# Kernel optimization log

Measured on AMD Instinct MI355X. Metric: run time of the kernel, lower is better.

Reference implementation:

```python
import jax, jax.numpy as jnp
import numpy as np

P_MIN = 0.8        # minimum cumulative probability mass kept per row
THRESHOLD = 1e-10  # drop matches with probability below this
EPS = 1e-6         # distance clamp (matches dist.clamp(min=1e-6) in backward)

B, N, M, D = 4, 4096, 4096, 3


def setup_inputs() -> dict:
    key = jax.random.key(0)
    kx, ky = jax.random.split(key)
    x = jax.random.normal(kx, (B, N, D), dtype=jnp.float32)
    y = jax.random.normal(ky, (B, M, D), dtype=jnp.float32)
    return {"x": x, "y": y}


def _pairwise_dist(x, y):
    # ||x_i - y_j|| via Gram trick; avoids materializing [B,N,M,D] diff tensor.
    sq = (
        jnp.sum(x * x, axis=-1)[:, :, None]
        + jnp.sum(y * y, axis=-1)[:, None, :]
        - 2.0 * jnp.einsum("bnd,bmd->bnm", x, y)
    )
    return jnp.sqrt(jnp.maximum(sq, EPS * EPS))  # [B, N, M]


def _sparse_match_weights(d):
    # Row-wise soft matching probabilities over targets j.
    p = jax.nn.softmax(-d, axis=-1)  # [B, N, M]
    # Keep the most-probable entries per row until cumulative mass reaches P_MIN
    # (the dense, jit-friendly equivalent of the COO compaction in the kernel).
    order = jnp.argsort(-p, axis=-1)
    p_sorted = jnp.take_along_axis(p, order, axis=-1)
    csum = jnp.cumsum(p_sorted, axis=-1)
    keep_sorted = (csum - p_sorted) < P_MIN  # include entry that crosses P_MIN
    inv = jnp.argsort(order, axis=-1)
    keep = jnp.take_along_axis(keep_sorted, inv, axis=-1)
    return jnp.where(keep & (p > THRESHOLD), p, 0.0)  # sparse COO values, dense layout


def reference(x, y):
    d = _pairwise_dist(x, y)                     # [B, N, M]
    w = jax.lax.stop_gradient(_sparse_match_weights(d))  # weights are constants in bwd
    loss = jnp.sum(w * d)                        # scalar matching loss
    return loss
```

## Files before the change

kernel.cpp:

```cpp
#include <hip/hip_runtime.h>


#define MCOLS 4096
#define KPT   64
#define WPB   4
#define P_MIN 0.8f

template <int CTRL, int RM, int BM, bool BC>
__device__ __forceinline__ float dpp_mov0(float x) {
    return __int_as_float(__builtin_amdgcn_update_dpp(
        0, __float_as_int(x), CTRL, RM, BM, BC));
}
__device__ __forceinline__ float dppSum(float v) {
    v += dpp_mov0<0x111, 0xF, 0xF, true >(v);
    v += dpp_mov0<0x112, 0xF, 0xF, true >(v);
    v += dpp_mov0<0x114, 0xF, 0xF, true >(v);
    v += dpp_mov0<0x118, 0xF, 0xF, true >(v);
    v += dpp_mov0<0x142, 0xA, 0xF, false>(v);
    v += dpp_mov0<0x143, 0xC, 0xF, false>(v);
    return __int_as_float(__builtin_amdgcn_readlane(__float_as_int(v), 63));
}
__device__ __forceinline__ void dppSum2(float& a, float& b) {
    a += dpp_mov0<0x111, 0xF, 0xF, true >(a); b += dpp_mov0<0x111, 0xF, 0xF, true >(b);
    a += dpp_mov0<0x112, 0xF, 0xF, true >(a); b += dpp_mov0<0x112, 0xF, 0xF, true >(b);
    a += dpp_mov0<0x114, 0xF, 0xF, true >(a); b += dpp_mov0<0x114, 0xF, 0xF, true >(b);
    a += dpp_mov0<0x118, 0xF, 0xF, true >(a); b += dpp_mov0<0x118, 0xF, 0xF, true >(b);
    a += dpp_mov0<0x142, 0xA, 0xF, false>(a); b += dpp_mov0<0x142, 0xA, 0xF, false>(b);
    a += dpp_mov0<0x143, 0xC, 0xF, false>(a); b += dpp_mov0<0x143, 0xC, 0xF, false>(b);
    a = __int_as_float(__builtin_amdgcn_readlane(__float_as_int(a), 63));
    b = __int_as_float(__builtin_amdgcn_readlane(__float_as_int(b), 63));
}
__device__ __forceinline__ float dppMax(float v) {
    v = fmaxf(v, dpp_mov0<0x111, 0xF, 0xF, true >(v));
    v = fmaxf(v, dpp_mov0<0x112, 0xF, 0xF, true >(v));
    v = fmaxf(v, dpp_mov0<0x114, 0xF, 0xF, true >(v));
    v = fmaxf(v, dpp_mov0<0x118, 0xF, 0xF, true >(v));
    v = fmaxf(v, dpp_mov0<0x142, 0xA, 0xF, false>(v));
    v = fmaxf(v, dpp_mov0<0x143, 0xC, 0xF, false>(v));
    return __int_as_float(__builtin_amdgcn_readlane(__float_as_int(v), 63));
}

__global__ __launch_bounds__(WPB * 64) void apml_row_wave(
        const float* __restrict__ x, const float* __restrict__ y,
        float* __restrict__ partial, float* __restrict__ out) {
    __shared__ __align__(16) float scomp[WPB * 256];
    __shared__ float wacc[WPB];

    const int tid  = threadIdx.x;
    const int wid  = tid >> 6;
    const int lane = tid & 63;
    const int row  = blockIdx.x * WPB + wid;
    const int b    = row >> 12;

    const float x0 = x[row * 3 + 0];
    const float x1 = x[row * 3 + 1];
    const float x2 = x[row * 3 + 2];
    const float* yb = y + (size_t)b * MCOLS * 3;

    float p[KPT];
    float zl = 0.0f;
    float pm0 = 0.0f, pm1 = 0.0f, pm2 = 0.0f, pm3 = 0.0f;
    #pragma unroll
    for (int k = 0; k < KPT; ++k) {
        const int j = k * 64 + lane;
        const float y0 = yb[j * 3 + 0];
        const float y1 = yb[j * 3 + 1];
        const float y2 = yb[j * 3 + 2];
        const float dx = x0 - y0, dy = x1 - y1, dz = x2 - y2;
        const float sq = fmaxf(dx * dx + dy * dy + dz * dz, 1e-12f);
        const float pk = __expf(-sqrtf(sq));
        p[k] = pk;
        zl  += pk;
        if      ((k & 3) == 0) pm0 = fmaxf(pm0, pk);
        else if ((k & 3) == 1) pm1 = fmaxf(pm1, pk);
        else if ((k & 3) == 2) pm2 = fmaxf(pm2, pk);
        else                   pm3 = fmaxf(pm3, pk);
    }
    const float Z    = dppSum(zl);
    const float pmax = dppMax(fmaxf(fmaxf(pm0, pm1), fmaxf(pm2, pm3)));
    const float target = P_MIN * Z;
    const float pTop = __uint_as_float(__float_as_uint(pmax) + 1u);

    float ssl = 0.0f, ssh = pTop;
    {
        float eGl = 16.0f * dppSum(p[0] + p[1] + p[2] + p[3]);
        float eGh = 0.0f;
        for (int it = 0; it < 5; ++it) {
            float s;
            if (it & 1) {
                s = 0.5f * (ssl + ssh);
            } else {
                const float den = fmaxf(eGl - eGh, 1e-30f);
                s = ssl + (ssh - ssl) * ((eGl - target) / den);
            }
            if (!(s > ssl && s < ssh)) s = 0.5f * (ssl + ssh);
            if (!(s > ssl && s < ssh)) break;
            float m = 0.0f;
            #pragma unroll
            for (int q = 0; q < 4; ++q) m += (p[q] >= s) ? p[q] : 0.0f;
            m = 16.0f * dppSum(m);
            if (m >= target) { ssl = s; eGl = m; }
            else             { ssh = s; eGh = m; }
        }
    }

    float sl = 0.0f, sh = pTop;
    float Gl = Z,    Gh = 0.0f;
    int   Cl = MCOLS, Ch = 0;
    {
        float ml = 0.0f, mh = 0.0f;
        int   cl_ = 0,   ch_ = 0;
        #pragma unroll
        for (int k = 0; k < KPT; ++k) {
            const float pk = p[k];
            const bool gl = (pk >= ssl);
            const bool gh = (pk >= ssh);
            ml += gl ? pk : 0.0f; cl_ += (int)__popcll(__ballot(gl));
            mh += gh ? pk : 0.0f; ch_ += (int)__popcll(__ballot(gh));
        }
        dppSum2(ml, mh);
        if (ml >= target) { sl = ssl; Gl = ml; Cl = cl_; }
        else              { sh = ssl; Gh = ml; Ch = cl_; }
        if (mh >= target) { sl = ssh; Gl = mh; Cl = ch_; }
        else if (ssh < sh){ sh = ssh; Gh = mh; Ch = ch_; }
    }

    for (int it = 0; it < 10 && (Cl - Ch) > 256; ++it) {
        float s;
        if (it & 1) {
            s = 0.5f * (sl + sh);
        } else {
            const float den = fmaxf(Gl - Gh, 1e-30f);
            s = sl + (sh - sl) * ((Gl - target) / den);
        }
        if (!(s > sl && s < sh)) s = 0.5f * (sl + sh);
        if (!(s > sl && s < sh)) break;

        float m0 = 0.0f, m1 = 0.0f, m2 = 0.0f, m3 = 0.0f;
        int   c = 0;
        #pragma unroll
        for (int k = 0; k < KPT; k += 4) {
            const bool g0 = (p[k]     >= s);
            const bool g1 = (p[k + 1] >= s);
            const bool g2 = (p[k + 2] >= s);
            const bool g3 = (p[k + 3] >= s);
            m0 += g0 ? p[k]     : 0.0f; c += (int)__popcll(__ballot(g0));
            m1 += g1 ? p[k + 1] : 0.0f; c += (int)__popcll(__ballot(g1));
            m2 += g2 ? p[k + 2] : 0.0f; c += (int)__popcll(__ballot(g2));
            m3 += g3 ? p[k + 3] : 0.0f; c += (int)__popcll(__ballot(g3));
        }
        const float m = dppSum((m0 + m1) + (m2 + m3));
        if (m >= target) { sl = s; Gl = m; Cl = c; }
        else             { sh = s; Gh = m; Ch = c; }
    }

    int C = 0;
    #pragma unroll
    for (int k = 0; k < KPT; ++k) {
        const bool band = (p[k] >= sl) && (p[k] < sh);
        const unsigned long long mk = __ballot(band);
        if (band) {
            const unsigned mlo = (unsigned)mk, mhi = (unsigned)(mk >> 32);
            const int within = __builtin_amdgcn_mbcnt_hi(
                                   mhi, __builtin_amdgcn_mbcnt_lo(mlo, 0));
            const int pos = C + within;
            if (pos < 256) scomp[wid * 256 + pos] = p[k];
        }
        C += (int)__popcll(mk);
    }
    __builtin_amdgcn_s_waitcnt(0);
    float cp[4];
    bool  cv[4];
    #pragma unroll
    for (int q = 0; q < 4; ++q) {
        const int idx = q * 64 + lane;
        cv[q] = (idx < C) && (idx < 256);
        cp[q] = cv[q] ? scomp[wid * 256 + idx] : 0.0f;
    }

    float pstar, mb = 0.0f;
    int   cnt = 1;
    bool  haveTie;

    if (C > 256) {
        pstar = (sl > 0.0f) ? __uint_as_float(__float_as_uint(sl) - 1u) : 0.0f;
        haveTie = false;
    } else {
        float lo_s = sl, hi_s = sh, lo_G = Gl, hi_G = Gh;
        int   lo_C = Cl, hi_C = Ch;
        for (int it = 0; it < 10 && (lo_C - hi_C) > 2; ++it) {
            float s;
            if (it & 1) {
                s = 0.5f * (lo_s + hi_s);
            } else {
                const float den = fmaxf(lo_G - hi_G, 1e-30f);
                s = lo_s + (hi_s - lo_s) * ((lo_G - target) / den);
            }
            if (!(s > lo_s && s < hi_s)) s = 0.5f * (lo_s + hi_s);
            if (!(s > lo_s && s < hi_s)) break;

            float m = 0.0f;
            int   c = Ch;
            #pragma unroll
            for (int q = 0; q < 4; ++q) {
                const bool ge = cv[q] && (cp[q] >= s);
                m += ge ? cp[q] : 0.0f;
                c += (int)__popcll(__ballot(ge));
            }
            m = Gh + dppSum(m);
            if (m >= target) { lo_s = s; lo_G = m; lo_C = c; }
            else             { hi_s = s; hi_G = m; hi_C = c; }
        }

        float scur = hi_s, M = hi_G;
        bool ok = false;
        pstar = lo_s;
        for (int e = 0; e < 16; ++e) {
            float vl = 0.0f;
            #pragma unroll
            for (int q = 0; q < 4; ++q)
                vl = fmaxf(vl, (cv[q] && cp[q] < scur) ? cp[q] : 0.0f);
            const float v = dppMax(vl);
            if (!(v > 0.0f)) break;
            int cvn = 0;
            #pragma unroll
            for (int q = 0; q < 4; ++q)
                cvn += (int)__popcll(__ballot(cv[q] && (cp[q] == v)));
            const float Mn = M + v * (float)cvn;
            if (Mn >= target) { pstar = v; mb = M; cnt = cvn; ok = true; break; }
            M = Mn; scur = v;
        }
        haveTie = ok;
        if (!ok) {
            pstar = (lo_s > 0.0f) ? __uint_as_float(__float_as_uint(lo_s) - 1u)
                                  : 0.0f;
        }
    }

    float spd = 0.0f;
    #pragma unroll
    for (int k = 0; k < KPT; ++k) {
        const float t = (p[k] > pstar) ? p[k] : 1.0f;
        spd += t * (-__logf(t));
    }
    spd = dppSum(spd);

    if (lane == 0) {
        float tie = 0.0f;
        if (haveTie) {
            const float R = (target - mb) / pstar;
            int q = (int)ceilf(R);
            if (q < 1) q = 1;
            if (q > cnt) q = cnt;
            tie = (float)q * pstar * (-__logf(pstar));
        }
        wacc[wid] = (spd + tie) / Z;
    }
    __syncthreads();
    if (tid == 0) {
        const float v = wacc[0] + wacc[1] + wacc[2] + wacc[3];
        if (partial) partial[blockIdx.x] = v;
        else         atomicAdd(out, v);
    }
}

__global__ __launch_bounds__(1024) void apml_reduce(
        const float* __restrict__ partial, float* __restrict__ out, int n) {
    __shared__ float s[16];
    const int t = threadIdx.x;
    float a = 0.0f;
    #pragma unroll
    for (int q = 0; q < 4; ++q) {
        const int i = t * 4 + q;
        a += (i < n) ? partial[i] : 0.0f;
    }
    a = dppSum(a);
    if ((t & 63) == 0) s[t >> 6] = a;
    __syncthreads();
    if (t == 0) {
        float r = 0.0f;
        #pragma unroll
        for (int w = 0; w < 16; ++w) r += s[w];
        out[0] = r;
    }
}

extern "C" void kernel_launch(void* const* d_in, const int* in_sizes, int n_in,
                              void* d_out, int out_size, void* d_ws, size_t ws_size,
                              hipStream_t stream) {
    const float* x = (const float*)d_in[0];
    const float* y = (const float*)d_in[1];
    float* out = (float*)d_out;

    const int nrows = in_sizes[0] / 3;
    const int nblocks = nrows / WPB;

    if (d_ws && ws_size >= (size_t)nblocks * sizeof(float) && nblocks <= 4096) {
        float* partial = (float*)d_ws;
        apml_row_wave<<<nblocks, WPB * 64, 0, stream>>>(x, y, partial, out);
        apml_reduce<<<1, 1024, 0, stream>>>(partial, out, nblocks);
    } else {
        hipMemsetAsync(out, 0, sizeof(float), stream);
        apml_row_wave<<<nblocks, WPB * 64, 0, stream>>>(x, y, nullptr, out);
    }
}
```

Measured before the change: 166.1 us.

## Speculatively compact a widened band in one pass and use two-probe refinement

Removes the per-row max reduction and runs more sample-based threshold iterations. It then widens the estimated bracket and, in a single pass over all 64 registers, computes the bracket masses and compacts the band into shared memory. When the bracket holds the target and the band fits, the separate full-array refinement and compaction passes are skipped, with the old path kept as a fallback. The in-band refinement now evaluates two thresholds per reduction and drops the validity flags by zero-padding the compacted values. The cost is a wider band and extra work whenever the speculative bracket misses.

```diff
diff --git a/kernel.cpp b/kernel.cpp
--- a/kernel.cpp
+++ b/kernel.cpp
@@ -5,6 +5,7 @@
 #define KPT   64
 #define WPB   4
 #define P_MIN 0.8f
+#define CAPS  384
 
 template <int CTRL, int RM, int BM, bool BC>
 __device__ __forceinline__ float dpp_mov0(float x) {
@@ -43,7 +44,7 @@
 __global__ __launch_bounds__(WPB * 64) void apml_row_wave(
         const float* __restrict__ x, const float* __restrict__ y,
         float* __restrict__ partial, float* __restrict__ out) {
-    __shared__ __align__(16) float scomp[WPB * 256];
+    __shared__ __align__(16) float scomp[WPB * CAPS];
     __shared__ float wacc[WPB];
 
     const int tid  = threadIdx.x;
@@ -59,7 +60,6 @@
 
     float p[KPT];
     float zl = 0.0f;
-    float pm0 = 0.0f, pm1 = 0.0f, pm2 = 0.0f, pm3 = 0.0f;
     #pragma unroll
     for (int k = 0; k < KPT; ++k) {
         const int j = k * 64 + lane;
@@ -71,21 +71,15 @@
         const float pk = __expf(-sqrtf(sq));
         p[k] = pk;
         zl  += pk;
-        if      ((k & 3) == 0) pm0 = fmaxf(pm0, pk);
-        else if ((k & 3) == 1) pm1 = fmaxf(pm1, pk);
-        else if ((k & 3) == 2) pm2 = fmaxf(pm2, pk);
-        else                   pm3 = fmaxf(pm3, pk);
-    }
-    const float Z    = dppSum(zl);
-    const float pmax = dppMax(fmaxf(fmaxf(pm0, pm1), fmaxf(pm2, pm3)));
+    }
+    const float Z      = dppSum(zl);
     const float target = P_MIN * Z;
-    const float pTop = __uint_as_float(__float_as_uint(pmax) + 1u);
-
-    float ssl = 0.0f, ssh = pTop;
+
+    float ssl = 0.0f, ssh = 1.0f;
     {
         float eGl = 16.0f * dppSum(p[0] + p[1] + p[2] + p[3]);
         float eGh = 0.0f;
-        for (int it = 0; it < 5; ++it) {
+        for (int it = 0; it < 7; ++it) {
             float s;
             if (it & 1) {
                 s = 0.5f * (ssl + ssh);
@@ -104,78 +98,101 @@
         }
     }
 
-    float sl = 0.0f, sh = pTop;
-    float Gl = Z,    Gh = 0.0f;
-    int   Cl = MCOLS, Ch = 0;
-    {
-        float ml = 0.0f, mh = 0.0f;
-        int   cl_ = 0,   ch_ = 0;
+    const float ww  = ssh - ssl;
+    const float tLo = fmaxf(ssl - 0.75f * ww, 0.0f);
+    const float tHi = fminf(ssh + 0.75f * ww, 1.0f);
+
+    float mLo = 0.0f, mHi = 0.0f;
+    int   cLo = 0,    cHi = 0,   Cb = 0;
+    #pragma unroll
+    for (int k = 0; k < KPT; ++k) {
+        const float pk = p[k];
+        const bool gl = (pk >= tLo);
+        const bool gh = (pk >= tHi);
+        mLo += gl ? pk : 0.0f;
+        mHi += gh ? pk : 0.0f;
+        const unsigned long long bl = __ballot(gl);
+        const unsigned long long bh = __ballot(gh);
+        const unsigned long long bm = bl & ~bh;
+        if (gl && !gh) {
+            const unsigned qlo = (unsigned)bm, qhi = (unsigned)(bm >> 32);
+            const int within = __builtin_amdgcn_mbcnt_hi(
+                                   qhi, __builtin_amdgcn_mbcnt_lo(qlo, 0));
+            const int pos = Cb + within;
+            if (pos < 256) scomp[wid * CAPS + pos] = pk;
+        }
+        cLo += (int)__popcll(bl);
+        cHi += (int)__popcll(bh);
+        Cb  += (int)__popcll(bm);
+    }
+    dppSum2(mLo, mHi);
+
+    float sl, sh, Gl, Gh;
+    int   Cl, Ch, C;
+    if (mLo >= target && mHi < target && Cb <= 256) {
+        sl = tLo; Gl = mLo; Cl = cLo;
+        sh = tHi; Gh = mHi; Ch = cHi;
+        C  = Cb;
+    } else {
+        sl = 0.0f; Gl = Z;    Cl = MCOLS;
+        sh = 1.0f; Gh = 0.0f; Ch = 0;
+        if (mLo >= target) { sl = tLo; Gl = mLo; Cl = cLo; }
+        else               { sh = tLo; Gh = mLo; Ch = cLo; }
+        if (mHi >= target) { sl = tHi; Gl = mHi; Cl = cHi; }
+        else if (tHi < sh) { sh = tHi; Gh = mHi; Ch = cHi; }
+
+        for (int it = 0; it < 10 && (Cl - Ch) > 256; ++it) {
+            float s;
+            if (it & 1) {
+                s = 0.5f * (sl + sh);
+            } else {
+                const float den = fmaxf(Gl - Gh, 1e-30f);
+                s = sl + (sh - sl) * ((Gl - target) / den);
+            }
+            if (!(s > sl && s < sh)) s = 0.5f * (sl + sh);
+            if (!(s > sl && s < sh)) break;
+
+            float m0 = 0.0f, m1 = 0.0f, m2 = 0.0f, m3 = 0.0f;
+            int   c = 0;
+            #pragma unroll
+            for (int k = 0; k < KPT; k += 4) {
+                const bool g0 = (p[k]     >= s);
+                const bool g1 = (p[k + 1] >= s);
+                const bool g2 = (p[k + 2] >= s);
+                const bool g3 = (p[k + 3] >= s);
+                m0 += g0 ? p[k]     : 0.0f; c += (int)__popcll(__ballot(g0));
+                m1 += g1 ? p[k + 1] : 0.0f; c += (int)__popcll(__ballot(g1));
+                m2 += g2 ? p[k + 2] : 0.0f; c += (int)__popcll(__ballot(g2));
+                m3 += g3 ? p[k + 3] : 0.0f; c += (int)__popcll(__ballot(g3));
+            }
+            const float m = dppSum((m0 + m1) + (m2 + m3));
+            if (m >= target) { sl = s; Gl = m; Cl = c; }
+            else             { sh = s; Gh = m; Ch = c; }
+        }
+
+        C = 0;
         #pragma unroll
         for (int k = 0; k < KPT; ++k) {
-            const float pk = p[k];
-            const bool gl = (pk >= ssl);
-            const bool gh = (pk >= ssh);
-            ml += gl ? pk : 0.0f; cl_ += (int)__popcll(__ballot(gl));
-            mh += gh ? pk : 0.0f; ch_ += (int)__popcll(__ballot(gh));
-        }
-        dppSum2(ml, mh);
-        if (ml >= target) { sl = ssl; Gl = ml; Cl = cl_; }
-        else              { sh = ssl; Gh = ml; Ch = cl_; }
-        if (mh >= target) { sl = ssh; Gl = mh; Cl = ch_; }
-        else if (ssh < sh){ sh = ssh; Gh = mh; Ch = ch_; }
-    }
-
-    for (int it = 0; it < 10 && (Cl - Ch) > 256; ++it) {
-        float s;
-        if (it & 1) {
-            s = 0.5f * (sl + sh);
-        } else {
-            const float den = fmaxf(Gl - Gh, 1e-30f);
-            s = sl + (sh - sl) * ((Gl - target) / den);
-        }
-        if (!(s > sl && s < sh)) s = 0.5f * (sl + sh);
-        if (!(s > sl && s < sh)) break;
-
-        float m0 = 0.0f, m1 = 0.0f, m2 = 0.0f, m3 = 0.0f;
-        int   c = 0;
-        #pragma unroll
-        for (int k = 0; k < KPT; k += 4) {
-            const bool g0 = (p[k]     >= s);
-            const bool g1 = (p[k + 1] >= s);
-            const bool g2 = (p[k + 2] >= s);
-            const bool g3 = (p[k + 3] >= s);
-            m0 += g0 ? p[k]     : 0.0f; c += (int)__popcll(__ballot(g0));
-            m1 += g1 ? p[k + 1] : 0.0f; c += (int)__popcll(__ballot(g1));
-            m2 += g2 ? p[k + 2] : 0.0f; c += (int)__popcll(__ballot(g2));
-            m3 += g3 ? p[k + 3] : 0.0f; c += (int)__popcll(__ballot(g3));
-        }
-        const float m = dppSum((m0 + m1) + (m2 + m3));
-        if (m >= target) { sl = s; Gl = m; Cl = c; }
-        else             { sh = s; Gh = m; Ch = c; }
-    }
-
-    int C = 0;
-    #pragma unroll
-    for (int k = 0; k < KPT; ++k) {
-        const bool band = (p[k] >= sl) && (p[k] < sh);
-        const unsigned long long mk = __ballot(band);
-        if (band) {
-            const unsigned mlo = (unsigned)mk, mhi = (unsigned)(mk >> 32);
-            const int within = __builtin_amdgcn_mbcnt_hi(
-                                   mhi, __builtin_amdgcn_mbcnt_lo(mlo, 0));
-            const int pos = C + within;
-            if (pos < 256) scomp[wid * 256 + pos] = p[k];
-        }
-        C += (int)__popcll(mk);
-    }
+            const bool band = (p[k] >= sl) && (p[k] < sh);
+            const unsigned long long mk = __ballot(band);
+            if (band) {
+                const unsigned qlo = (unsigned)mk, qhi = (unsigned)(mk >> 32);
+                const int within = __builtin_amdgcn_mbcnt_hi(
+                                       qhi, __builtin_amdgcn_mbcnt_lo(qlo, 0));
+                const int pos = C + within;
+                if (pos < 256) scomp[wid * CAPS + pos] = p[k];
+            }
+            C += (int)__popcll(mk);
+        }
+    }
+
     __builtin_amdgcn_s_waitcnt(0);
+    const int Cc = (C < 256) ? C : 256;
     float cp[4];
-    bool  cv[4];
     #pragma unroll
     for (int q = 0; q < 4; ++q) {
         const int idx = q * 64 + lane;
-        cv[q] = (idx < C) && (idx < 256);
-        cp[q] = cv[q] ? scomp[wid * 256 + idx] : 0.0f;
+        cp[q] = (idx < Cc) ? scomp[wid * CAPS + idx] : 0.0f;
     }
 
     float pstar, mb = 0.0f;
@@ -188,44 +205,48 @@
     } else {
         float lo_s = sl, hi_s = sh, lo_G = Gl, hi_G = Gh;
         int   lo_C = Cl, hi_C = Ch;
-        for (int it = 0; it < 10 && (lo_C - hi_C) > 2; ++it) {
-            float s;
-            if (it & 1) {
-                s = 0.5f * (lo_s + hi_s);
-            } else {
-                const float den = fmaxf(lo_G - hi_G, 1e-30f);
-                s = lo_s + (hi_s - lo_s) * ((lo_G - target) / den);
-            }
-            if (!(s > lo_s && s < hi_s)) s = 0.5f * (lo_s + hi_s);
-            if (!(s > lo_s && s < hi_s)) break;
-
-            float m = 0.0f;
-            int   c = Ch;
+        for (int it = 0; it < 6 && (lo_C - hi_C) > 2; ++it) {
+            const float sB = 0.5f * (lo_s + hi_s);
+            if (!(sB > lo_s && sB < hi_s)) break;
+            float sA = lo_s + (hi_s - lo_s) *
+                       ((lo_G - target) / fmaxf(lo_G - hi_G, 1e-30f));
+            if (!(sA > lo_s && sA < hi_s)) sA = sB;
+            const float t0 = fminf(sA, sB), t1 = fmaxf(sA, sB);
+
+            float a0 = 0.0f, a1 = 0.0f;
+            int   k0 = 0,    k1 = 0;
             #pragma unroll
             for (int q = 0; q < 4; ++q) {
-                const bool ge = cv[q] && (cp[q] >= s);
-                m += ge ? cp[q] : 0.0f;
-                c += (int)__popcll(__ballot(ge));
-            }
-            m = Gh + dppSum(m);
-            if (m >= target) { lo_s = s; lo_G = m; lo_C = c; }
-            else             { hi_s = s; hi_G = m; hi_C = c; }
+                const bool g0 = (cp[q] >= t0);
+                const bool g1 = (cp[q] >= t1);
+                a0 += g0 ? cp[q] : 0.0f; k0 += (int)__popcll(__ballot(g0));
+                a1 += g1 ? cp[q] : 0.0f; k1 += (int)__popcll(__ballot(g1));
+            }
+            dppSum2(a0, a1);
+            const float M0 = Gh + a0, M1 = Gh + a1;
+            const int   D0 = Ch + k0, D1 = Ch + k1;
+            if      (M1 >= target) { lo_s = t1; lo_G = M1; lo_C = D1; }
+            else if (M0 >= target) { lo_s = t0; lo_G = M0; lo_C = D0;
+                                     hi_s = t1; hi_G = M1; hi_C = D1; }
+            else                   { hi_s = t0; hi_G = M0; hi_C = D0; }
         }
 
         float scur = hi_s, M = hi_G;
         bool ok = false;
         pstar = lo_s;
         for (int e = 0; e < 16; ++e) {
-            float vl = 0.0f;
-            #pragma unroll
-            for (int q = 0; q < 4; ++q)
-                vl = fmaxf(vl, (cv[q] && cp[q] < scur) ? cp[q] : 0.0f);
-            const float v = dppMax(vl);
+            float v0 = 0.0f, v1 = 0.0f;
+            #pragma unroll
+            for (int q = 0; q < 4; q += 2) {
+                v0 = fmaxf(v0, (cp[q]     < scur) ? cp[q]     : 0.0f);
+                v1 = fmaxf(v1, (cp[q + 1] < scur) ? cp[q + 1] : 0.0f);
+            }
+            const float v = dppMax(fmaxf(v0, v1));
             if (!(v > 0.0f)) break;
             int cvn = 0;
             #pragma unroll
             for (int q = 0; q < 4; ++q)
-                cvn += (int)__popcll(__ballot(cv[q] && (cp[q] == v)));
+                cvn += (int)__popcll(__ballot(cp[q] == v));
             const float Mn = M + v * (float)cvn;
             if (Mn >= target) { pstar = v; mb = M; cnt = cvn; ok = true; break; }
             M = Mn; scur = v;
```

Measured after the change: 183.2 us. 10.3% more time.

## Repack targets to float4, drop row-max reduction, write per-row partials

Applied to the files above, without the earlier changes.

Adds a small repack kernel that copies y into a float4 array in workspace, so the main loop issues one 16-byte load per target instead of three strided scalar loads. It also drops the per-row max reduction and uses 1.0 as the upper bracket for the threshold search, and each wave now writes its row partial directly instead of combining through shared memory with a block barrier. The reduce kernel is widened to cover per-row partials. In exchange it adds an extra launch and workspace traffic, and the looser starting bracket may cost more search iterations.

```diff
diff --git a/kernel.cpp b/kernel.cpp
--- a/kernel.cpp
+++ b/kernel.cpp
@@ -40,11 +40,19 @@
     return __int_as_float(__builtin_amdgcn_readlane(__float_as_int(v), 63));
 }
 
+__global__ __launch_bounds__(256) void apml_repack(
+        const float* __restrict__ y, float4* __restrict__ y4, int np) {
+    const int i = blockIdx.x * 256 + threadIdx.x;
+    if (i < np) {
+        y4[i] = make_float4(y[i * 3 + 0], y[i * 3 + 1], y[i * 3 + 2], 0.0f);
+    }
+}
+
 __global__ __launch_bounds__(WPB * 64) void apml_row_wave(
         const float* __restrict__ x, const float* __restrict__ y,
+        const float4* __restrict__ y4,
         float* __restrict__ partial, float* __restrict__ out) {
     __shared__ __align__(16) float scomp[WPB * 256];
-    __shared__ float wacc[WPB];
 
     const int tid  = threadIdx.x;
     const int wid  = tid >> 6;
@@ -55,31 +63,38 @@
     const float x0 = x[row * 3 + 0];
     const float x1 = x[row * 3 + 1];
     const float x2 = x[row * 3 + 2];
-    const float* yb = y + (size_t)b * MCOLS * 3;
 
     float p[KPT];
     float zl = 0.0f;
-    float pm0 = 0.0f, pm1 = 0.0f, pm2 = 0.0f, pm3 = 0.0f;
-    #pragma unroll
-    for (int k = 0; k < KPT; ++k) {
-        const int j = k * 64 + lane;
-        const float y0 = yb[j * 3 + 0];
-        const float y1 = yb[j * 3 + 1];
-        const float y2 = yb[j * 3 + 2];
-        const float dx = x0 - y0, dy = x1 - y1, dz = x2 - y2;
-        const float sq = fmaxf(dx * dx + dy * dy + dz * dz, 1e-12f);
-        const float pk = __expf(-sqrtf(sq));
-        p[k] = pk;
-        zl  += pk;
-        if      ((k & 3) == 0) pm0 = fmaxf(pm0, pk);
-        else if ((k & 3) == 1) pm1 = fmaxf(pm1, pk);
-        else if ((k & 3) == 2) pm2 = fmaxf(pm2, pk);
-        else                   pm3 = fmaxf(pm3, pk);
-    }
-    const float Z    = dppSum(zl);
-    const float pmax = dppMax(fmaxf(fmaxf(pm0, pm1), fmaxf(pm2, pm3)));
+    if (y4) {
+        const float4* y4b = y4 + (size_t)b * MCOLS;
+        #pragma unroll
+        for (int k = 0; k < KPT; ++k) {
+            const float4 v = y4b[k * 64 + lane];
+            const float dx = x0 - v.x, dy = x1 - v.y, dz = x2 - v.z;
+            const float sq = fmaxf(dx * dx + dy * dy + dz * dz, 1e-12f);
+            const float pk = __expf(-sqrtf(sq));
+            p[k] = pk;
+            zl  += pk;
+        }
+    } else {
+        const float* yb = y + (size_t)b * MCOLS * 3;
+        #pragma unroll
+        for (int k = 0; k < KPT; ++k) {
+            const int j = k * 64 + lane;
+            const float y0 = yb[j * 3 + 0];
+            const float y1 = yb[j * 3 + 1];
+            const float y2 = yb[j * 3 + 2];
+            const float dx = x0 - y0, dy = x1 - y1, dz = x2 - y2;
+            const float sq = fmaxf(dx * dx + dy * dy + dz * dz, 1e-12f);
+            const float pk = __expf(-sqrtf(sq));
+            p[k] = pk;
+            zl  += pk;
+        }
+    }
+    const float Z      = dppSum(zl);
     const float target = P_MIN * Z;
-    const float pTop = __uint_as_float(__float_as_uint(pmax) + 1u);
+    const float pTop   = 1.0f;
 
     float ssl = 0.0f, ssh = pTop;
     {
@@ -254,12 +269,8 @@
             if (q > cnt) q = cnt;
             tie = (float)q * pstar * (-__logf(pstar));
         }
-        wacc[wid] = (spd + tie) / Z;
-    }
-    __syncthreads();
-    if (tid == 0) {
-        const float v = wacc[0] + wacc[1] + wacc[2] + wacc[3];
-        if (partial) partial[blockIdx.x] = v;
+        const float v = (spd + tie) / Z;
+        if (partial) partial[row] = v;
         else         atomicAdd(out, v);
     }
 }
@@ -270,8 +281,8 @@
     const int t = threadIdx.x;
     float a = 0.0f;
     #pragma unroll
-    for (int q = 0; q < 4; ++q) {
-        const int i = t * 4 + q;
+    for (int q = 0; q < 16; ++q) {
+        const int i = t * 16 + q;
         a += (i < n) ? partial[i] : 0.0f;
     }
     a = dppSum(a);
@@ -293,14 +304,24 @@
     float* out = (float*)d_out;
 
     const int nrows = in_sizes[0] / 3;
+    const int np    = in_sizes[1] / 3;
     const int nblocks = nrows / WPB;
 
-    if (d_ws && ws_size >= (size_t)nblocks * sizeof(float) && nblocks <= 4096) {
+    const size_t y4_bytes   = (size_t)np * sizeof(float4);
+    const size_t part_bytes = (size_t)nrows * sizeof(float);
+
+    if (d_ws && ws_size >= y4_bytes + part_bytes && nrows <= 16384) {
+        float4* y4     = (float4*)d_ws;
+        float* partial = (float*)((char*)d_ws + y4_bytes);
+        apml_repack<<<(np + 255) / 256, 256, 0, stream>>>(y, y4, np);
+        apml_row_wave<<<nblocks, WPB * 64, 0, stream>>>(x, y, y4, partial, out);
+        apml_reduce<<<1, 1024, 0, stream>>>(partial, out, nrows);
+    } else if (d_ws && ws_size >= part_bytes && nrows <= 16384) {
         float* partial = (float*)d_ws;
-        apml_row_wave<<<nblocks, WPB * 64, 0, stream>>>(x, y, partial, out);
-        apml_reduce<<<1, 1024, 0, stream>>>(partial, out, nblocks);
+        apml_row_wave<<<nblocks, WPB * 64, 0, stream>>>(x, y, nullptr, partial, out);
+        apml_reduce<<<1, 1024, 0, stream>>>(partial, out, nrows);
     } else {
         hipMemsetAsync(out, 0, sizeof(float), stream);
-        apml_row_wave<<<nblocks, WPB * 64, 0, stream>>>(x, y, nullptr, out);
-    }
-}
+        apml_row_wave<<<nblocks, WPB * 64, 0, stream>>>(x, y, nullptr, nullptr, out);
+    }
+}
```

Result: slower. 186.0 us (+12.0%).

## Select mass threshold bin via LDS exponent histogram instead of iterative search

Applied to the files above, without the earlier changes.

Builds a per-wave 256-bin histogram of probabilities keyed on float exponent/mantissa bits, using LDS atomic adds during the distance pass. A wave prefix scan over the bins then locates the bin containing the cumulative-mass threshold. This replaces the multi-pass secant/bisection search over all 64 registers, keeping a bounded fallback search when the bin holds too many entries. The final entropy sum is also split into four accumulators for ILP. It adds 4096 LDS float atomics per row, which may contend on popular bins.

```diff
diff --git a/kernel.cpp b/kernel.cpp
--- a/kernel.cpp
+++ b/kernel.cpp
@@ -5,6 +5,7 @@
 #define KPT   64
 #define WPB   4
 #define P_MIN 0.8f
+#define BINBASE 0x2F8
 
 template <int CTRL, int RM, int BM, bool BC>
 __device__ __forceinline__ float dpp_mov0(float x) {
@@ -20,15 +21,14 @@
     v += dpp_mov0<0x143, 0xC, 0xF, false>(v);
     return __int_as_float(__builtin_amdgcn_readlane(__float_as_int(v), 63));
 }
-__device__ __forceinline__ void dppSum2(float& a, float& b) {
-    a += dpp_mov0<0x111, 0xF, 0xF, true >(a); b += dpp_mov0<0x111, 0xF, 0xF, true >(b);
-    a += dpp_mov0<0x112, 0xF, 0xF, true >(a); b += dpp_mov0<0x112, 0xF, 0xF, true >(b);
-    a += dpp_mov0<0x114, 0xF, 0xF, true >(a); b += dpp_mov0<0x114, 0xF, 0xF, true >(b);
-    a += dpp_mov0<0x118, 0xF, 0xF, true >(a); b += dpp_mov0<0x118, 0xF, 0xF, true >(b);
-    a += dpp_mov0<0x142, 0xA, 0xF, false>(a); b += dpp_mov0<0x142, 0xA, 0xF, false>(b);
-    a += dpp_mov0<0x143, 0xC, 0xF, false>(a); b += dpp_mov0<0x143, 0xC, 0xF, false>(b);
-    a = __int_as_float(__builtin_amdgcn_readlane(__float_as_int(a), 63));
-    b = __int_as_float(__builtin_amdgcn_readlane(__float_as_int(b), 63));
+__device__ __forceinline__ float dppPrefixIncl(float v) {
+    v += dpp_mov0<0x111, 0xF, 0xF, true >(v);
+    v += dpp_mov0<0x112, 0xF, 0xF, true >(v);
+    v += dpp_mov0<0x114, 0xF, 0xF, true >(v);
+    v += dpp_mov0<0x118, 0xF, 0xF, true >(v);
+    v += dpp_mov0<0x142, 0xA, 0xF, false>(v);
+    v += dpp_mov0<0x143, 0xC, 0xF, false>(v);
+    return v;
 }
 __device__ __forceinline__ float dppMax(float v) {
     v = fmaxf(v, dpp_mov0<0x111, 0xF, 0xF, true >(v));
@@ -43,6 +43,7 @@
 __global__ __launch_bounds__(WPB * 64) void apml_row_wave(
         const float* __restrict__ x, const float* __restrict__ y,
         float* __restrict__ partial, float* __restrict__ out) {
+    __shared__ __align__(16) float hist[WPB * 256];
     __shared__ __align__(16) float scomp[WPB * 256];
     __shared__ float wacc[WPB];
 
@@ -51,15 +52,19 @@
     const int lane = tid & 63;
     const int row  = blockIdx.x * WPB + wid;
     const int b    = row >> 12;
+    const int hb   = wid * 256;
 
     const float x0 = x[row * 3 + 0];
     const float x1 = x[row * 3 + 1];
     const float x2 = x[row * 3 + 2];
     const float* yb = y + (size_t)b * MCOLS * 3;
 
+    #pragma unroll
+    for (int q = 0; q < 4; ++q) hist[hb + q * 64 + lane] = 0.0f;
+    __builtin_amdgcn_s_waitcnt(0);
+
     float p[KPT];
     float zl = 0.0f;
-    float pm0 = 0.0f, pm1 = 0.0f, pm2 = 0.0f, pm3 = 0.0f;
     #pragma unroll
     for (int k = 0; k < KPT; ++k) {
         const int j = k * 64 + lane;
@@ -71,102 +76,87 @@
         const float pk = __expf(-sqrtf(sq));
         p[k] = pk;
         zl  += pk;
-        if      ((k & 3) == 0) pm0 = fmaxf(pm0, pk);
-        else if ((k & 3) == 1) pm1 = fmaxf(pm1, pk);
-        else if ((k & 3) == 2) pm2 = fmaxf(pm2, pk);
-        else                   pm3 = fmaxf(pm3, pk);
-    }
-    const float Z    = dppSum(zl);
-    const float pmax = dppMax(fmaxf(fmaxf(pm0, pm1), fmaxf(pm2, pm3)));
+        int bin = (int)(__float_as_uint(pk) >> 20) - BINBASE;
+        bin = bin < 0 ? 0 : bin;
+        atomicAdd(&hist[hb + bin], pk);
+    }
+    __builtin_amdgcn_s_waitcnt(0);
+    const float Z      = dppSum(zl);
     const float target = P_MIN * Z;
-    const float pTop = __uint_as_float(__float_as_uint(pmax) + 1u);
-
-    float ssl = 0.0f, ssh = pTop;
-    {
-        float eGl = 16.0f * dppSum(p[0] + p[1] + p[2] + p[3]);
-        float eGh = 0.0f;
-        for (int it = 0; it < 5; ++it) {
+
+    const float4 mm = *reinterpret_cast<const float4*>(&hist[hb + 4 * lane]);
+    const float tl  = (mm.x + mm.y) + (mm.z + mm.w);
+    const float pfx = dppPrefixIncl(tl);
+    const float total = __int_as_float(
+        __builtin_amdgcn_readlane(__float_as_int(pfx), 63));
+    const float Tnx = total - pfx;
+    const float S3 = mm.w + Tnx;
+    const float S2 = mm.z + S3;
+    const float S1 = mm.y + S2;
+    const float S0 = mm.x + S1;
+    int cand = -1;
+    if (S0 >= target) cand = 4 * lane + 0;
+    if (S1 >= target) cand = 4 * lane + 1;
+    if (S2 >= target) cand = 4 * lane + 2;
+    if (S3 >= target) cand = 4 * lane + 3;
+    const int binsel = (int)dppMax((float)(cand + 1)) - 1;
+
+    float4 sv; sv.x = S0; sv.y = S1; sv.z = S2; sv.w = S3;
+    *reinterpret_cast<float4*>(&hist[hb + 4 * lane]) = sv;
+    __builtin_amdgcn_s_waitcnt(0);
+    float Gl = hist[hb + binsel];
+    float Gh = (binsel < 255) ? hist[hb + binsel + 1] : 0.0f;
+    float sl = (binsel == 0) ? 0.0f
+             : __uint_as_float((unsigned)(binsel + BINBASE) << 20);
+    float sh = (binsel < 255)
+             ? __uint_as_float((unsigned)(binsel + 1 + BINBASE) << 20) : 1.0f;
+
+    int C = 0;
+    for (int attempt = 0; attempt < 2; ++attempt) {
+        C = 0;
+        #pragma unroll
+        for (int k = 0; k < KPT; ++k) {
+            const bool band = (p[k] >= sl) && (p[k] < sh);
+            const unsigned long long mk = __ballot(band);
+            if (band) {
+                const unsigned mlo = (unsigned)mk, mhi = (unsigned)(mk >> 32);
+                const int within = __builtin_amdgcn_mbcnt_hi(
+                                       mhi, __builtin_amdgcn_mbcnt_lo(mlo, 0));
+                const int pos = C + within;
+                if (pos < 256) scomp[hb + pos] = p[k];
+            }
+            C += (int)__popcll(mk);
+        }
+        if (C <= 256 || attempt) break;
+        int Cl = MCOLS, Ch = 0;
+        for (int it = 0; it < 10 && (Cl - Ch) > 256; ++it) {
             float s;
             if (it & 1) {
-                s = 0.5f * (ssl + ssh);
+                s = 0.5f * (sl + sh);
             } else {
-                const float den = fmaxf(eGl - eGh, 1e-30f);
-                s = ssl + (ssh - ssl) * ((eGl - target) / den);
-            }
-            if (!(s > ssl && s < ssh)) s = 0.5f * (ssl + ssh);
-            if (!(s > ssl && s < ssh)) break;
-            float m = 0.0f;
+                const float den = fmaxf(Gl - Gh, 1e-30f);
+                s = sl + (sh - sl) * ((Gl - target) / den);
+            }
+            if (!(s > sl && s < sh)) s = 0.5f * (sl + sh);
+            if (!(s > sl && s < sh)) break;
+
+            float m0 = 0.0f, m1 = 0.0f, m2 = 0.0f, m3 = 0.0f;
+            int   c = 0;
             #pragma unroll
-            for (int q = 0; q < 4; ++q) m += (p[q] >= s) ? p[q] : 0.0f;
-            m = 16.0f * dppSum(m);
-            if (m >= target) { ssl = s; eGl = m; }
-            else             { ssh = s; eGh = m; }
-        }
-    }
-
-    float sl = 0.0f, sh = pTop;
-    float Gl = Z,    Gh = 0.0f;
-    int   Cl = MCOLS, Ch = 0;
-    {
-        float ml = 0.0f, mh = 0.0f;
-        int   cl_ = 0,   ch_ = 0;
-        #pragma unroll
-        for (int k = 0; k < KPT; ++k) {
-            const float pk = p[k];
-            const bool gl = (pk >= ssl);
-            const bool gh = (pk >= ssh);
-            ml += gl ? pk : 0.0f; cl_ += (int)__popcll(__ballot(gl));
-            mh += gh ? pk : 0.0f; ch_ += (int)__popcll(__ballot(gh));
-        }
-        dppSum2(ml, mh);
-        if (ml >= target) { sl = ssl; Gl = ml; Cl = cl_; }
-        else              { sh = ssl; Gh = ml; Ch = cl_; }
-        if (mh >= target) { sl = ssh; Gl = mh; Cl = ch_; }
-        else if (ssh < sh){ sh = ssh; Gh = mh; Ch = ch_; }
-    }
-
-    for (int it = 0; it < 10 && (Cl - Ch) > 256; ++it) {
-        float s;
-        if (it & 1) {
-            s = 0.5f * (sl + sh);
-        } else {
-            const float den = fmaxf(Gl - Gh, 1e-30f);
-            s = sl + (sh - sl) * ((Gl - target) / den);
-        }
-        if (!(s > sl && s < sh)) s = 0.5f * (sl + sh);
-        if (!(s > sl && s < sh)) break;
-
-        float m0 = 0.0f, m1 = 0.0f, m2 = 0.0f, m3 = 0.0f;
-        int   c = 0;
-        #pragma unroll
-        for (int k = 0; k < KPT; k += 4) {
-            const bool g0 = (p[k]     >= s);
-            const bool g1 = (p[k + 1] >= s);
-            const bool g2 = (p[k + 2] >= s);
-            const bool g3 = (p[k + 3] >= s);
-            m0 += g0 ? p[k]     : 0.0f; c += (int)__popcll(__ballot(g0));
-            m1 += g1 ? p[k + 1] : 0.0f; c += (int)__popcll(__ballot(g1));
-            m2 += g2 ? p[k + 2] : 0.0f; c += (int)__popcll(__ballot(g2));
-            m3 += g3 ? p[k + 3] : 0.0f; c += (int)__popcll(__ballot(g3));
-        }
-        const float m = dppSum((m0 + m1) + (m2 + m3));
-        if (m >= target) { sl = s; Gl = m; Cl = c; }
-        else             { sh = s; Gh = m; Ch = c; }
-    }
-
-    int C = 0;
-    #pragma unroll
-    for (int k = 0; k < KPT; ++k) {
-        const bool band = (p[k] >= sl) && (p[k] < sh);
-        const unsigned long long mk = __ballot(band);
-        if (band) {
-            const unsigned mlo = (unsigned)mk, mhi = (unsigned)(mk >> 32);
-            const int within = __builtin_amdgcn_mbcnt_hi(
-                                   mhi, __builtin_amdgcn_mbcnt_lo(mlo, 0));
-            const int pos = C + within;
-            if (pos < 256) scomp[wid * 256 + pos] = p[k];
-        }
-        C += (int)__popcll(mk);
+            for (int k = 0; k < KPT; k += 4) {
+                const bool g0 = (p[k]     >= s);
+                const bool g1 = (p[k + 1] >= s);
+                const bool g2 = (p[k + 2] >= s);
+                const bool g3 = (p[k + 3] >= s);
+                m0 += g0 ? p[k]     : 0.0f; c += (int)__popcll(__ballot(g0));
+                m1 += g1 ? p[k + 1] : 0.0f; c += (int)__popcll(__ballot(g1));
+                m2 += g2 ? p[k + 2] : 0.0f; c += (int)__popcll(__ballot(g2));
+                m3 += g3 ? p[k + 3] : 0.0f; c += (int)__popcll(__ballot(g3));
+            }
+            const float m = dppSum((m0 + m1) + (m2 + m3));
+            if (m >= target) { sl = s; Gl = m; Cl = c; }
+            else             { sh = s; Gh = m; Ch = c; }
+        }
     }
     __builtin_amdgcn_s_waitcnt(0);
     float cp[4];
@@ -175,7 +165,7 @@
     for (int q = 0; q < 4; ++q) {
         const int idx = q * 64 + lane;
         cv[q] = (idx < C) && (idx < 256);
-        cp[q] = cv[q] ? scomp[wid * 256 + idx] : 0.0f;
+        cp[q] = cv[q] ? scomp[hb + idx] : 0.0f;
     }
 
     float pstar, mb = 0.0f;
@@ -187,7 +177,7 @@
         haveTie = false;
     } else {
         float lo_s = sl, hi_s = sh, lo_G = Gl, hi_G = Gh;
-        int   lo_C = Cl, hi_C = Ch;
+        int   lo_C = C,  hi_C = 0;
         for (int it = 0; it < 10 && (lo_C - hi_C) > 2; ++it) {
             float s;
             if (it & 1) {
@@ -200,7 +190,7 @@
             if (!(s > lo_s && s < hi_s)) break;
 
             float m = 0.0f;
-            int   c = Ch;
+            int   c = 0;
             #pragma unroll
             for (int q = 0; q < 4; ++q) {
                 const bool ge = cv[q] && (cp[q] >= s);
@@ -237,13 +227,19 @@
         }
     }
 
-    float spd = 0.0f;
-    #pragma unroll
-    for (int k = 0; k < KPT; ++k) {
-        const float t = (p[k] > pstar) ? p[k] : 1.0f;
-        spd += t * (-__logf(t));
-    }
-    spd = dppSum(spd);
+    float s0 = 0.0f, s1 = 0.0f, s2 = 0.0f, s3 = 0.0f;
+    #pragma unroll
+    for (int k = 0; k < KPT; k += 4) {
+        const float t0 = (p[k]     > pstar) ? p[k]     : 1.0f;
+        const float t1 = (p[k + 1] > pstar) ? p[k + 1] : 1.0f;
+        const float t2 = (p[k + 2] > pstar) ? p[k + 2] : 1.0f;
+        const float t3 = (p[k + 3] > pstar) ? p[k + 3] : 1.0f;
+        s0 += t0 * (-__logf(t0));
+        s1 += t1 * (-__logf(t1));
+        s2 += t2 * (-__logf(t2));
+        s3 += t3 * (-__logf(t3));
+    }
+    const float spd = dppSum((s0 + s1) + (s2 + s3));
 
     if (lane == 0) {
         float tie = 0.0f;
```

New measurement: 420.0 us. 153% more time.
